# Kernel tuning notes

Hardware: AMD Instinct MI355X
Metric: run time of the kernel (lower is better)

Reference implementation:

```python
import jax, jax.numpy as jnp
import numpy as np

EMBED_DIM = 1024
HEADS = 16
HEAD_DIM = EMBED_DIM // HEADS


def setup_inputs() -> dict:
    key = jax.random.key(0)
    k1, k2, k3, k4 = jax.random.split(key, 4)
    x = jax.random.normal(k1, (4, 2048, EMBED_DIM), dtype=jnp.float32)
    # nn.Linear weights stored as (out, in); apply as x @ W.T
    W_qkv = jax.random.normal(k2, (3 * EMBED_DIM, EMBED_DIM), dtype=jnp.float32) / np.sqrt(EMBED_DIM)
    W_out = jax.random.normal(k3, (EMBED_DIM, EMBED_DIM), dtype=jnp.float32) / np.sqrt(EMBED_DIM)
    b_out = jax.random.normal(k4, (EMBED_DIM,), dtype=jnp.float32) * 0.02
    return {"x": x, "W_qkv": W_qkv, "W_out": W_out, "b_out": b_out}


def reference(x, W_qkv, W_out, b_out):
    B, N, _ = x.shape
    qkv = jnp.einsum('bnd,ed->bne', x, W_qkv)  # (B, N, 3*E)
    q, k, v = jnp.split(qkv, 3, axis=-1)
    # (B, H, N, Dh)
    q = q.reshape(B, N, HEADS, HEAD_DIM).transpose(0, 2, 1, 3)
    k = k.reshape(B, N, HEADS, HEAD_DIM).transpose(0, 2, 1, 3)
    v = v.reshape(B, N, HEADS, HEAD_DIM).transpose(0, 2, 1, 3)
    scale = 1.0 / np.sqrt(HEAD_DIM).astype(np.float32)
    scores = jnp.einsum('bhqd,bhkd->bhqk', q, k) * scale  # (B, H, N, N)
    attn = jax.nn.softmax(scores, axis=-1)
    out = jnp.einsum('bhqk,bhkd->bhqd', attn, v)  # (B, H, N, Dh)
    out = out.transpose(0, 2, 1, 3).reshape(B, N, EMBED_DIM)
    return jnp.einsum('bne,oe->bno', out, W_out) + b_out
```

## Files before the change

kernel.cpp:

```cpp
#include <hip/hip_runtime.h>
#include <hip/hip_bf16.h>
#include <stdint.h>


typedef _Float16 half8 __attribute__((ext_vector_type(8)));
typedef __fp16 fp16x2 __attribute__((ext_vector_type(2)));
typedef float floatx4 __attribute__((ext_vector_type(4)));

#define E 1024
#define NH 16
#define DH 64
#define SEQ 2048
#define BATCH 4

__device__ __forceinline__ void gload_lds16(const void* g, void* lds) {
  typedef __attribute__((address_space(1))) void gv;
  typedef __attribute__((address_space(3))) void lv;
  __builtin_amdgcn_global_load_lds((gv*)g, (lv*)lds, 16, 0, 0);
}

__device__ __forceinline__ float fast_exp2(float x) {
#if __has_builtin(__builtin_amdgcn_exp2f)
  return __builtin_amdgcn_exp2f(x);
#else
  return exp2f(x);
#endif
}

__global__ __launch_bounds__(256)
void cvt3_f32_f16(const float* __restrict__ a, _Float16* __restrict__ oa, int na,
                  const float* __restrict__ b, _Float16* __restrict__ ob, int nb,
                  const float* __restrict__ c, _Float16* __restrict__ oc, int nc) {
  int i = blockIdx.x * 256 + threadIdx.x;
  const float* in;
  _Float16* out;
  int idx;
  if (i < na) { in = a; out = oa; idx = i; }
  else if (i < na + nb) { in = b; out = ob; idx = i - na; }
  else if (i < na + nb + nc) { in = c; out = oc; idx = i - na - nb; }
  else return;
  const float4* p = (const float4*)in;
  float4 u = p[2 * idx], v = p[2 * idx + 1];
  half8 h;
  h[0] = (_Float16)u.x; h[1] = (_Float16)u.y; h[2] = (_Float16)u.z; h[3] = (_Float16)u.w;
  h[4] = (_Float16)v.x; h[5] = (_Float16)v.y; h[6] = (_Float16)v.z; h[7] = (_Float16)v.w;
  ((half8*)out)[idx] = h;
}

__global__ __launch_bounds__(256)
void gemm_qkv(const _Float16* __restrict__ A, const _Float16* __restrict__ W,
              _Float16* __restrict__ qo, _Float16* __restrict__ ko, _Float16* __restrict__ vo) {
  __shared__ __align__(16) _Float16 As[128 * 64];
  __shared__ __align__(16) _Float16 Bs[128 * 64];
  const int t = threadIdx.x;
  const int w = t >> 6, l = t & 63;
  const int wr = w >> 1, wc = w & 1;
  const int lr = l & 15, hi = l >> 4;
  const int tileRow = blockIdx.y * 128;
  const int tileCol = blockIdx.x * 128;
  const int ldsW = (t & ~63) * 16;
  floatx4 acc[4][4] = {};

  for (int k0 = 0; k0 < 1024; k0 += 64) {
    __syncthreads();
#pragma unroll
    for (int c = 0; c < 4; ++c) {
      int idx = c * 256 + t;
      int row = idx >> 3, g = idx & 7;
      gload_lds16(A + (size_t)(tileRow + row) * 1024 + k0 + g * 8, (char*)As + c * 4096 + ldsW);
      gload_lds16(W + (size_t)(tileCol + row) * 1024 + k0 + g * 8, (char*)Bs + c * 4096 + ldsW);
    }
    __syncthreads();
#pragma unroll
    for (int kk = 0; kk < 2; ++kk) {
      half8 af[4], bf[4];
#pragma unroll
      for (int m = 0; m < 4; ++m)
        af[m] = *(const half8*)(As + (wr * 64 + m * 16 + lr) * 64 + kk * 32 + hi * 8);
#pragma unroll
      for (int n = 0; n < 4; ++n)
        bf[n] = *(const half8*)(Bs + (wc * 64 + n * 16 + lr) * 64 + kk * 32 + hi * 8);
#pragma unroll
      for (int m = 0; m < 4; ++m)
#pragma unroll
        for (int n = 0; n < 4; ++n)
          acc[m][n] = __builtin_amdgcn_mfma_f32_16x16x32_f16(af[m], bf[n], acc[m][n], 0, 0, 0);
    }
  }
  const int sec = tileCol >> 10;
  _Float16* dst = sec == 0 ? qo : (sec == 1 ? ko : vo);
  const float scaleq = sec == 0 ? 0.18033688011112042f : 1.0f;
  const int b = tileRow >> 11;
  const int tokBase = (tileRow & 2047) + wr * 64;
#pragma unroll
  for (int n = 0; n < 4; ++n) {
    int col = (tileCol & 1023) + wc * 64 + n * 16 + lr;
    int h = col >> 6, d = col & 63;
    _Float16* base = dst + (((size_t)b * NH + h) * SEQ + tokBase) * DH + d;
#pragma unroll
    for (int m = 0; m < 4; ++m)
#pragma unroll
      for (int j = 0; j < 4; ++j)
        base[(size_t)(m * 16 + hi * 4 + j) * DH] = (_Float16)(acc[m][n][j] * scaleq);
  }
}

__global__ __launch_bounds__(256)
void transpose_v(const _Float16* __restrict__ V, _Float16* __restrict__ VT) {
  __shared__ __align__(16) _Float16 L[64][80];
  const int bh = blockIdx.y, tt = blockIdx.x;
  const int t = threadIdx.x;
  const _Float16* vb = V + ((size_t)bh * SEQ + tt * 64) * DH;
#pragma unroll
  for (int c = 0; c < 2; ++c) {
    int idx = c * 256 + t;
    int row = idx >> 3, d0 = (idx & 7) * 8;
    *(half8*)&L[row][d0] = *(const half8*)(vb + row * DH + d0);
  }
  __syncthreads();
  _Float16* ob = VT + (size_t)bh * DH * SEQ + tt * 64;
#pragma unroll
  for (int c = 0; c < 2; ++c) {
    int idx = c * 256 + t;
    int d = idx >> 3, k0 = (idx & 7) * 8;
    half8 x;
#pragma unroll
    for (int jj = 0; jj < 8; ++jj) x[jj] = L[k0 + jj][d];
    *(half8*)(ob + (size_t)d * SEQ + k0) = x;
  }
}

__global__ __launch_bounds__(256)
void attn(const _Float16* __restrict__ Q, const _Float16* __restrict__ Kg,
          const _Float16* __restrict__ VT, _Float16* __restrict__ O) {
  __shared__ __align__(16) _Float16 Ks[2][64 * 64];
  __shared__ __align__(16) _Float16 Vs[2][64 * 64];
  __shared__ __align__(16) _Float16 Ps[4][16 * 64];
  const int bh = blockIdx.y, qt = blockIdx.x;
  const int t = threadIdx.x, w = t >> 6, l = t & 63;
  const int lr = l & 15, hi = l >> 4;
  const int ldsW = (t & ~63) * 16;
  const _Float16* qb = Q + ((size_t)bh * SEQ + qt * 64 + w * 16) * DH;
  half8 qf[2];
  qf[0] = *(const half8*)(qb + lr * DH + hi * 8);
  qf[1] = *(const half8*)(qb + lr * DH + 32 + hi * 8);
  floatx4 o_acc[4] = {};
  float m_run = 0.f, l_run = 0.f;
  const _Float16* kb = Kg + (size_t)bh * SEQ * DH;
  const _Float16* vb = VT + (size_t)bh * DH * SEQ;
  char* pw = (char*)&Ps[w][0];
  const int lrm = lr & 7;
  uint32_t wra[4], rda[2];
#pragma unroll
  for (int n = 0; n < 4; ++n)
    wra[n] = lr * 128 + ((((2 * n + (hi >> 1)) ^ lrm)) << 4) + (hi & 1) * 8;
#pragma unroll
  for (int kk = 0; kk < 2; ++kk)
    rda[kk] = lr * 128 + (((4 * kk + hi) ^ lrm) << 4);

  auto stage = [&](int kt, int b) {
#pragma unroll
    for (int c = 0; c < 2; ++c) {
      int idx = c * 256 + t;
      int row = idx >> 3, g = idx & 7, gs = g ^ (row & 7);
      gload_lds16(kb + (size_t)(kt * 64 + row) * DH + gs * 8, (char*)Ks[b] + c * 4096 + ldsW);
      gload_lds16(vb + (size_t)row * SEQ + kt * 64 + gs * 8, (char*)Vs[b] + c * 4096 + ldsW);
    }
  };

  stage(0, 0);
  __syncthreads();
  int buf = 0;
  for (int kt = 0; kt < SEQ / 64; ++kt) {
    if (kt + 1 < SEQ / 64) stage(kt + 1, buf ^ 1);
    floatx4 cb = {-m_run, -m_run, -m_run, -m_run};
    floatx4 s[4] = {cb, cb, cb, cb};
    __builtin_amdgcn_s_setprio(1);
#pragma unroll
    for (int kk = 0; kk < 2; ++kk) {
      int gl = kk * 4 + hi;
#pragma unroll
      for (int n = 0; n < 4; ++n) {
        int key = n * 16 + lr;
        half8 af = *(const half8*)((char*)Ks[buf] + key * 128 + ((gl ^ (key & 7)) << 4));
        s[n] = __builtin_amdgcn_mfma_f32_16x16x32_f16(af, qf[kk], s[n], 0, 0, 0);
      }
    }
    __builtin_amdgcn_s_setprio(0);
    float m01 = fmaxf(fmaxf(s[0][0], s[0][1]), fmaxf(s[0][2], s[0][3]));
    float m23 = fmaxf(fmaxf(s[1][0], s[1][1]), fmaxf(s[1][2], s[1][3]));
    float m45 = fmaxf(fmaxf(s[2][0], s[2][1]), fmaxf(s[2][2], s[2][3]));
    float m67 = fmaxf(fmaxf(s[3][0], s[3][1]), fmaxf(s[3][2], s[3][3]));
    float mx = fmaxf(fmaxf(m01, m23), fmaxf(m45, m67));
    mx = fmaxf(mx, __shfl_xor(mx, 16));
    mx = fmaxf(mx, __shfl_xor(mx, 32));
    fp16x2 pk[4][2];
    float rs;
    if (__builtin_expect(__any(mx > 10.f), 0)) {
      float dm = fmaxf(mx, 0.f);
      float fac = fast_exp2(-dm);
      m_run += dm;
      l_run *= fac;
#pragma unroll
      for (int j = 0; j < 4; ++j) {
        float fj = __shfl(fac, hi * 4 + j);
#pragma unroll
        for (int n = 0; n < 4; ++n) o_acc[n][j] *= fj;
      }
      rs = 0.f;
#pragma unroll
      for (int n = 0; n < 4; ++n) {
        float p0 = fast_exp2(s[n][0] - dm), p1 = fast_exp2(s[n][1] - dm);
        float p2 = fast_exp2(s[n][2] - dm), p3 = fast_exp2(s[n][3] - dm);
        pk[n][0] = __builtin_amdgcn_cvt_pkrtz(p0, p1);
        pk[n][1] = __builtin_amdgcn_cvt_pkrtz(p2, p3);
        rs += p0 + p1 + p2 + p3;
      }
    } else {
      rs = 0.f;
#pragma unroll
      for (int n = 0; n < 4; ++n) {
        float p0 = fast_exp2(s[n][0]), p1 = fast_exp2(s[n][1]);
        float p2 = fast_exp2(s[n][2]), p3 = fast_exp2(s[n][3]);
        pk[n][0] = __builtin_amdgcn_cvt_pkrtz(p0, p1);
        pk[n][1] = __builtin_amdgcn_cvt_pkrtz(p2, p3);
        rs += p0 + p1 + p2 + p3;
      }
    }
    l_run += rs;
#pragma unroll
    for (int n = 0; n < 4; ++n) {
      uint2 v;
      v.x = __builtin_bit_cast(uint32_t, pk[n][0]);
      v.y = __builtin_bit_cast(uint32_t, pk[n][1]);
      *(uint2*)(pw + wra[n]) = v;
    }
    half8 pf[2];
    pf[0] = *(const half8*)(pw + rda[0]);
    pf[1] = *(const half8*)(pw + rda[1]);
    __builtin_amdgcn_s_setprio(1);
#pragma unroll
    for (int kk = 0; kk < 2; ++kk) {
      int gl = kk * 4 + hi;
#pragma unroll
      for (int n = 0; n < 4; ++n) {
        int d = n * 16 + lr;
        half8 vf = *(const half8*)((char*)Vs[buf] + d * 128 + ((gl ^ (d & 7)) << 4));
        o_acc[n] = __builtin_amdgcn_mfma_f32_16x16x32_f16(pf[kk], vf, o_acc[n], 0, 0, 0);
      }
    }
    __builtin_amdgcn_s_setprio(0);
    __syncthreads();
    buf ^= 1;
  }
  l_run += __shfl_xor(l_run, 16);
  l_run += __shfl_xor(l_run, 32);
  const int b = bh >> 4, h = bh & 15;
#pragma unroll
  for (int j = 0; j < 4; ++j) {
    float lj = __shfl(l_run, hi * 4 + j);
    float inv = 1.f / lj;
    int tok = qt * 64 + w * 16 + hi * 4 + j;
    _Float16* ob = O + ((size_t)b * SEQ + tok) * E + h * DH;
#pragma unroll
    for (int n = 0; n < 4; ++n) ob[n * 16 + lr] = (_Float16)(o_acc[n][j] * inv);
  }
}

__global__ __launch_bounds__(256)
void gemm_out(const _Float16* __restrict__ A, const _Float16* __restrict__ W,
              const float* __restrict__ bias, float* __restrict__ out) {
  __shared__ __align__(16) _Float16 As[128 * 64];
  __shared__ __align__(16) _Float16 Bs[128 * 64];
  const int t = threadIdx.x;
  const int w = t >> 6, l = t & 63;
  const int wr = w >> 1, wc = w & 1;
  const int lr = l & 15, hi = l >> 4;
  const int tileRow = blockIdx.y * 128;
  const int tileCol = blockIdx.x * 128;
  const int ldsW = (t & ~63) * 16;
  floatx4 acc[4][4] = {};

  for (int k0 = 0; k0 < 1024; k0 += 64) {
    __syncthreads();
#pragma unroll
    for (int c = 0; c < 4; ++c) {
      int idx = c * 256 + t;
      int row = idx >> 3, g = idx & 7;
      gload_lds16(A + (size_t)(tileRow + row) * 1024 + k0 + g * 8, (char*)As + c * 4096 + ldsW);
      gload_lds16(W + (size_t)(tileCol + row) * 1024 + k0 + g * 8, (char*)Bs + c * 4096 + ldsW);
    }
    __syncthreads();
#pragma unroll
    for (int kk = 0; kk < 2; ++kk) {
      half8 af[4], bf[4];
#pragma unroll
      for (int m = 0; m < 4; ++m)
        af[m] = *(const half8*)(As + (wr * 64 + m * 16 + lr) * 64 + kk * 32 + hi * 8);
#pragma unroll
      for (int n = 0; n < 4; ++n)
        bf[n] = *(const half8*)(Bs + (wc * 64 + n * 16 + lr) * 64 + kk * 32 + hi * 8);
#pragma unroll
      for (int m = 0; m < 4; ++m)
#pragma unroll
        for (int n = 0; n < 4; ++n)
          acc[m][n] = __builtin_amdgcn_mfma_f32_16x16x32_f16(af[m], bf[n], acc[m][n], 0, 0, 0);
    }
  }
#pragma unroll
  for (int n = 0; n < 4; ++n) {
    int col = tileCol + wc * 64 + n * 16 + lr;
    float bv = bias[col];
#pragma unroll
    for (int m = 0; m < 4; ++m) {
      int row = tileRow + wr * 64 + m * 16 + hi * 4;
#pragma unroll
      for (int j = 0; j < 4; ++j)
        out[(size_t)(row + j) * E + col] = acc[m][n][j] + bv;
    }
  }
}

extern "C" void kernel_launch(void* const* d_in, const int* in_sizes, int n_in,
                              void* d_out, int out_size, void* d_ws, size_t ws_size,
                              hipStream_t stream) {
  const float* x = (const float*)d_in[0];
  const float* Wqkv = (const float*)d_in[1];
  const float* Wout = (const float*)d_in[2];
  const float* bout = (const float*)d_in[3];
  float* out = (float*)d_out;
  char* ws = (char*)d_ws;
  _Float16* x16 = (_Float16*)(ws);
  _Float16* q16 = (_Float16*)(ws + (16u << 20));
  _Float16* k16 = (_Float16*)(ws + (32u << 20));
  _Float16* v16 = (_Float16*)(ws + (48u << 20));
  _Float16* wq16 = (_Float16*)(ws + (64u << 20));
  _Float16* wo16 = (_Float16*)(ws + (70u << 20));
  _Float16* vt16 = x16;
  _Float16* ao16 = v16;

  int n8x = in_sizes[0] / 8, n8q = in_sizes[1] / 8, n8o = in_sizes[2] / 8;
  int n8 = n8x + n8q + n8o;
  cvt3_f32_f16<<<(n8 + 255) / 256, 256, 0, stream>>>(x, x16, n8x, Wqkv, wq16, n8q, Wout, wo16, n8o);
  gemm_qkv<<<dim3(24, 64), 256, 0, stream>>>(x16, wq16, q16, k16, v16);
  transpose_v<<<dim3(32, 64), 256, 0, stream>>>(v16, vt16);
  attn<<<dim3(32, 64), 256, 0, stream>>>(q16, k16, vt16, ao16);
  gemm_out<<<dim3(8, 64), 256, 0, stream>>>(ao16, wo16, bout, out);
}
```

Measured before the change: 263.5 us.

## Process two query groups per wave in attention, single-buffer K/V tiles

The attention kernel now gives each wave 32 query rows instead of 16, handled as two 16-row groups. Each K/V tile loaded into shared memory is reused for twice as many queries, which halves the grid and the total K/V traffic. The K/V double buffer is replaced by one buffer with two barriers per step, K/V fragments are hoisted into registers, and launch bounds request 3 blocks per CU to recover overlap across blocks. The softmax of group 1 is interleaved with the PV MFMAs of group 0. Removing the prefetch exposes load latency within each block, and the extra registers may limit occupancy.

```diff
diff --git a/kernel.cpp b/kernel.cpp
--- a/kernel.cpp
+++ b/kernel.cpp
@@ -25,6 +25,10 @@
 #else
   return exp2f(x);
 #endif
+}
+
+__device__ __forceinline__ float max3f(float a, float b, float c) {
+  return fmaxf(fmaxf(a, b), c);
 }
 
 __global__ __launch_bounds__(256)
@@ -130,22 +134,25 @@
   }
 }
 
-__global__ __launch_bounds__(256)
+__global__ __launch_bounds__(256, 3)
 void attn(const _Float16* __restrict__ Q, const _Float16* __restrict__ Kg,
           const _Float16* __restrict__ VT, _Float16* __restrict__ O) {
-  __shared__ __align__(16) _Float16 Ks[2][64 * 64];
-  __shared__ __align__(16) _Float16 Vs[2][64 * 64];
+  __shared__ __align__(16) _Float16 Ks[64 * 64];
+  __shared__ __align__(16) _Float16 Vs[64 * 64];
   __shared__ __align__(16) _Float16 Ps[4][16 * 64];
   const int bh = blockIdx.y, qt = blockIdx.x;
   const int t = threadIdx.x, w = t >> 6, l = t & 63;
   const int lr = l & 15, hi = l >> 4;
   const int ldsW = (t & ~63) * 16;
-  const _Float16* qb = Q + ((size_t)bh * SEQ + qt * 64 + w * 16) * DH;
-  half8 qf[2];
-  qf[0] = *(const half8*)(qb + lr * DH + hi * 8);
-  qf[1] = *(const half8*)(qb + lr * DH + 32 + hi * 8);
-  floatx4 o_acc[4] = {};
-  float m_run = 0.f, l_run = 0.f;
+  const _Float16* qb = Q + ((size_t)bh * SEQ + qt * 128 + w * 32) * DH;
+  half8 qf[2][2];
+#pragma unroll
+  for (int g = 0; g < 2; ++g) {
+    qf[g][0] = *(const half8*)(qb + (g * 16 + lr) * DH + hi * 8);
+    qf[g][1] = *(const half8*)(qb + (g * 16 + lr) * DH + 32 + hi * 8);
+  }
+  floatx4 o0[4] = {}, o1[4] = {};
+  float m0 = 0.f, m1 = 0.f, l0 = 0.f, l1 = 0.f;
   const _Float16* kb = Kg + (size_t)bh * SEQ * DH;
   const _Float16* vb = VT + (size_t)bh * DH * SEQ;
   char* pw = (char*)&Ps[w][0];
@@ -158,56 +165,27 @@
   for (int kk = 0; kk < 2; ++kk)
     rda[kk] = lr * 128 + (((4 * kk + hi) ^ lrm) << 4);
 
-  auto stage = [&](int kt, int b) {
-#pragma unroll
-    for (int c = 0; c < 2; ++c) {
-      int idx = c * 256 + t;
-      int row = idx >> 3, g = idx & 7, gs = g ^ (row & 7);
-      gload_lds16(kb + (size_t)(kt * 64 + row) * DH + gs * 8, (char*)Ks[b] + c * 4096 + ldsW);
-      gload_lds16(vb + (size_t)row * SEQ + kt * 64 + gs * 8, (char*)Vs[b] + c * 4096 + ldsW);
-    }
-  };
-
-  stage(0, 0);
-  __syncthreads();
-  int buf = 0;
-  for (int kt = 0; kt < SEQ / 64; ++kt) {
-    if (kt + 1 < SEQ / 64) stage(kt + 1, buf ^ 1);
-    floatx4 cb = {-m_run, -m_run, -m_run, -m_run};
-    floatx4 s[4] = {cb, cb, cb, cb};
-    __builtin_amdgcn_s_setprio(1);
-#pragma unroll
-    for (int kk = 0; kk < 2; ++kk) {
-      int gl = kk * 4 + hi;
-#pragma unroll
-      for (int n = 0; n < 4; ++n) {
-        int key = n * 16 + lr;
-        half8 af = *(const half8*)((char*)Ks[buf] + key * 128 + ((gl ^ (key & 7)) << 4));
-        s[n] = __builtin_amdgcn_mfma_f32_16x16x32_f16(af, qf[kk], s[n], 0, 0, 0);
-      }
-    }
-    __builtin_amdgcn_s_setprio(0);
-    float m01 = fmaxf(fmaxf(s[0][0], s[0][1]), fmaxf(s[0][2], s[0][3]));
-    float m23 = fmaxf(fmaxf(s[1][0], s[1][1]), fmaxf(s[1][2], s[1][3]));
-    float m45 = fmaxf(fmaxf(s[2][0], s[2][1]), fmaxf(s[2][2], s[2][3]));
-    float m67 = fmaxf(fmaxf(s[3][0], s[3][1]), fmaxf(s[3][2], s[3][3]));
-    float mx = fmaxf(fmaxf(m01, m23), fmaxf(m45, m67));
+  auto sm = [&](floatx4(&s)[4], float& mr, float& lsum, floatx4(&oa)[4], fp16x2(&pk)[4][2]) {
+    float ma = max3f(s[0][0], s[0][1], s[0][2]);
+    float mb = max3f(s[0][3], s[1][0], s[1][1]);
+    float mc = max3f(s[1][2], s[1][3], s[2][0]);
+    float md = max3f(s[2][1], s[2][2], s[2][3]);
+    float me = max3f(s[3][0], s[3][1], s[3][2]);
+    float mx = max3f(max3f(ma, mb, mc), fmaxf(md, me), s[3][3]);
     mx = fmaxf(mx, __shfl_xor(mx, 16));
     mx = fmaxf(mx, __shfl_xor(mx, 32));
-    fp16x2 pk[4][2];
-    float rs;
+    float rs = 0.f;
     if (__builtin_expect(__any(mx > 10.f), 0)) {
       float dm = fmaxf(mx, 0.f);
       float fac = fast_exp2(-dm);
-      m_run += dm;
-      l_run *= fac;
+      mr += dm;
+      lsum *= fac;
 #pragma unroll
       for (int j = 0; j < 4; ++j) {
         float fj = __shfl(fac, hi * 4 + j);
 #pragma unroll
-        for (int n = 0; n < 4; ++n) o_acc[n][j] *= fj;
-      }
-      rs = 0.f;
+        for (int n = 0; n < 4; ++n) oa[n][j] *= fj;
+      }
 #pragma unroll
       for (int n = 0; n < 4; ++n) {
         float p0 = fast_exp2(s[n][0] - dm), p1 = fast_exp2(s[n][1] - dm);
@@ -217,7 +195,6 @@
         rs += p0 + p1 + p2 + p3;
       }
     } else {
-      rs = 0.f;
 #pragma unroll
       for (int n = 0; n < 4; ++n) {
         float p0 = fast_exp2(s[n][0]), p1 = fast_exp2(s[n][1]);
@@ -227,7 +204,10 @@
         rs += p0 + p1 + p2 + p3;
       }
     }
-    l_run += rs;
+    lsum += rs;
+  };
+
+  auto proute = [&](fp16x2(&pk)[4][2], half8(&pf)[2]) {
 #pragma unroll
     for (int n = 0; n < 4; ++n) {
       uint2 v;
@@ -235,35 +215,91 @@
       v.y = __builtin_bit_cast(uint32_t, pk[n][1]);
       *(uint2*)(pw + wra[n]) = v;
     }
-    half8 pf[2];
     pf[0] = *(const half8*)(pw + rda[0]);
     pf[1] = *(const half8*)(pw + rda[1]);
-    __builtin_amdgcn_s_setprio(1);
+  };
+
+  for (int kt = 0; kt < SEQ / 64; ++kt) {
+    __syncthreads();
+#pragma unroll
+    for (int c = 0; c < 2; ++c) {
+      int idx = c * 256 + t;
+      int row = idx >> 3, g = idx & 7, gs = g ^ (row & 7);
+      gload_lds16(kb + (size_t)(kt * 64 + row) * DH + gs * 8, (char*)Ks + c * 4096 + ldsW);
+      gload_lds16(vb + (size_t)row * SEQ + kt * 64 + gs * 8, (char*)Vs + c * 4096 + ldsW);
+    }
+    __syncthreads();
+    half8 af[8];
 #pragma unroll
     for (int kk = 0; kk < 2; ++kk) {
       int gl = kk * 4 + hi;
 #pragma unroll
       for (int n = 0; n < 4; ++n) {
+        int key = n * 16 + lr;
+        af[kk * 4 + n] = *(const half8*)((char*)Ks + key * 128 + ((gl ^ (key & 7)) << 4));
+      }
+    }
+    floatx4 cb0 = {-m0, -m0, -m0, -m0}, cb1 = {-m1, -m1, -m1, -m1};
+    floatx4 s0[4] = {cb0, cb0, cb0, cb0}, s1[4] = {cb1, cb1, cb1, cb1};
+    __builtin_amdgcn_s_setprio(1);
+#pragma unroll
+    for (int kk = 0; kk < 2; ++kk)
+#pragma unroll
+      for (int n = 0; n < 4; ++n)
+        s0[n] = __builtin_amdgcn_mfma_f32_16x16x32_f16(af[kk * 4 + n], qf[0][kk], s0[n], 0, 0, 0);
+#pragma unroll
+    for (int kk = 0; kk < 2; ++kk)
+#pragma unroll
+      for (int n = 0; n < 4; ++n)
+        s1[n] = __builtin_amdgcn_mfma_f32_16x16x32_f16(af[kk * 4 + n], qf[1][kk], s1[n], 0, 0, 0);
+    __builtin_amdgcn_s_setprio(0);
+    fp16x2 pk[4][2];
+    half8 pf[2];
+    sm(s0, m0, l0, o0, pk);
+    proute(pk, pf);
+    half8 vf[8];
+#pragma unroll
+    for (int kk = 0; kk < 2; ++kk) {
+      int gl = kk * 4 + hi;
+#pragma unroll
+      for (int n = 0; n < 4; ++n) {
         int d = n * 16 + lr;
-        half8 vf = *(const half8*)((char*)Vs[buf] + d * 128 + ((gl ^ (d & 7)) << 4));
-        o_acc[n] = __builtin_amdgcn_mfma_f32_16x16x32_f16(pf[kk], vf, o_acc[n], 0, 0, 0);
-      }
-    }
+        vf[kk * 4 + n] = *(const half8*)((char*)Vs + d * 128 + ((gl ^ (d & 7)) << 4));
+      }
+    }
+    __builtin_amdgcn_s_setprio(1);
+#pragma unroll
+    for (int kk = 0; kk < 2; ++kk)
+#pragma unroll
+      for (int n = 0; n < 4; ++n)
+        o0[n] = __builtin_amdgcn_mfma_f32_16x16x32_f16(pf[kk], vf[kk * 4 + n], o0[n], 0, 0, 0);
     __builtin_amdgcn_s_setprio(0);
-    __syncthreads();
-    buf ^= 1;
-  }
-  l_run += __shfl_xor(l_run, 16);
-  l_run += __shfl_xor(l_run, 32);
+    sm(s1, m1, l1, o1, pk);
+    proute(pk, pf);
+    __builtin_amdgcn_s_setprio(1);
+#pragma unroll
+    for (int kk = 0; kk < 2; ++kk)
+#pragma unroll
+      for (int n = 0; n < 4; ++n)
+        o1[n] = __builtin_amdgcn_mfma_f32_16x16x32_f16(pf[kk], vf[kk * 4 + n], o1[n], 0, 0, 0);
+    __builtin_amdgcn_s_setprio(0);
+  }
+  l0 += __shfl_xor(l0, 16); l0 += __shfl_xor(l0, 32);
+  l1 += __shfl_xor(l1, 16); l1 += __shfl_xor(l1, 32);
   const int b = bh >> 4, h = bh & 15;
 #pragma unroll
-  for (int j = 0; j < 4; ++j) {
-    float lj = __shfl(l_run, hi * 4 + j);
-    float inv = 1.f / lj;
-    int tok = qt * 64 + w * 16 + hi * 4 + j;
-    _Float16* ob = O + ((size_t)b * SEQ + tok) * E + h * DH;
-#pragma unroll
-    for (int n = 0; n < 4; ++n) ob[n * 16 + lr] = (_Float16)(o_acc[n][j] * inv);
+  for (int g = 0; g < 2; ++g) {
+    const floatx4* oa = g == 0 ? o0 : o1;
+    float lg = g == 0 ? l0 : l1;
+#pragma unroll
+    for (int j = 0; j < 4; ++j) {
+      float lj = __shfl(lg, hi * 4 + j);
+      float inv = 1.f / lj;
+      int tok = qt * 128 + w * 32 + g * 16 + hi * 4 + j;
+      _Float16* ob = O + ((size_t)b * SEQ + tok) * E + h * DH;
+#pragma unroll
+      for (int n = 0; n < 4; ++n) ob[n * 16 + lr] = (_Float16)(oa[n][j] * inv);
+    }
   }
 }
 
@@ -344,6 +380,6 @@
   cvt3_f32_f16<<<(n8 + 255) / 256, 256, 0, stream>>>(x, x16, n8x, Wqkv, wq16, n8q, Wout, wo16, n8o);
   gemm_qkv<<<dim3(24, 64), 256, 0, stream>>>(x16, wq16, q16, k16, v16);
   transpose_v<<<dim3(32, 64), 256, 0, stream>>>(v16, vt16);
-  attn<<<dim3(32, 64), 256, 0, stream>>>(q16, k16, vt16, ao16);
+  attn<<<dim3(16, 64), 256, 0, stream>>>(q16, k16, vt16, ao16);
   gemm_out<<<dim3(8, 64), 256, 0, stream>>>(ao16, wo16, bout, out);
 }
```

Result: faster. 234.6 us (-11.0%).
